# Kernel tuning notes

Measured on AMD Instinct MI355X. Metric: run time of the kernel, lower is better.

Reference implementation:

```python
import jax, jax.numpy as jnp
import numpy as np

ALG_DIM = 248   # dim of E8 adjoint rep
NNZ = 30000     # number of nonzero structure constants f_{ij}^k
BATCH = 8192


def setup_inputs() -> dict:
    key = jax.random.key(0)
    k1, k2, k3, k4, k5, k6 = jax.random.split(key, 6)
    x = jax.random.normal(k1, (BATCH, ALG_DIM), dtype=jnp.float32)
    y = jax.random.normal(k2, (BATCH, ALG_DIM), dtype=jnp.float32)
    idx_i = jax.random.randint(k3, (NNZ,), 0, ALG_DIM, dtype=jnp.int32)
    idx_j = jax.random.randint(k4, (NNZ,), 0, ALG_DIM, dtype=jnp.int32)
    idx_k = jax.random.randint(k5, (NNZ,), 0, ALG_DIM, dtype=jnp.int32)
    coeff = jax.random.normal(k6, (NNZ,), dtype=jnp.float32)
    alpha = jnp.ones((1,), dtype=jnp.float32)
    return {"x": x, "y": y, "idx_i": idx_i, "idx_j": idx_j,
            "idx_k": idx_k, "coeff": coeff, "alpha": alpha}


def reference(x, y, idx_i, idx_j, idx_k, coeff, alpha):
    # Sparse Lie bracket via structure-constant triples:
    #   out[b, k] = sum_{t : idx_k[t]==k} coeff[t] * x[b, idx_i[t]] * y[b, idx_j[t]]
    vals = x[:, idx_i] * y[:, idx_j] * coeff[None, :]          # (B, nnz)
    bracket = jnp.zeros_like(x).at[:, idx_k].add(vals)          # (B, 248)
    return alpha[0] * bracket
```

## Files before the change

### kernel.cpp

```cpp
#include <hip/hip_runtime.h>

#define ALG_DIM 248
#define ROWS 32
#define KSPLIT 4
#define KPB 62
#define PMAX 1024
#define CB 16
#define PLSTRIDE_B 3984
#define PLSTRIDE_DW 996

typedef __fp16 h2v __attribute__((ext_vector_type(2)));
union H2U { unsigned u; h2v h; };


__global__ __launch_bounds__(1024) void k_prep(
    const int* __restrict__ idx_k, int* __restrict__ meta,
    int* __restrict__ perm, int* __restrict__ ssz,
    int* __restrict__ coff, int* __restrict__ glim,
    uint2* __restrict__ packedP, int nnz)
{
    __shared__ int h[CB * 256];
    __shared__ int sz[256];
    __shared__ int ssl[256];
    __shared__ int red[256];
    const int tid = threadIdx.x;

    for (int u = tid; u < CB * 256; u += 1024) h[u] = 0;
    __syncthreads();

    const int w = tid >> 6, lane = tid & 63;
    const int chunk = (nnz + CB - 1) / CB;
    const int lo = w * chunk, hi = min(nnz, lo + chunk);
    for (int t = lo + lane; t < hi; t += 64)
        atomicAdd(&h[(w << 8) + idx_k[t]], 1);
    __syncthreads();

    if (tid < 256) {
        int tot = 0;
        for (int b = 0; b < CB; ++b) tot += h[b * 256 + tid];
        sz[tid] = (tid < ALG_DIM) ? tot : 0;
        red[tid] = sz[tid];
    }
    __syncthreads();
    for (int off = 128; off > 0; off >>= 1) {
        if (tid < off) red[tid] = max(red[tid], red[tid + off]);
        __syncthreads();
    }
    int P = (red[0] + 7) & ~7;
    P = max(P, 8);
    P = min(P, PMAX);
    if (tid == 0) meta[0] = P;
    const int stride = P + 8;

    int rank = 0, mysz = 0;
    if (tid < ALG_DIM) {
        mysz = sz[tid];
        for (int k = 0; k < ALG_DIM; ++k) {
            int s2 = sz[k];
            rank += (s2 > mysz) || (s2 == mysz && k < tid);
        }
        perm[rank] = tid;
        ssz[rank]  = mysz;
        ssl[rank]  = mysz;
        const int base = rank * stride;
        glim[tid] = base + P;
        int run = base;
        for (int b = 0; b < CB; ++b) {
            coff[b * 256 + tid] = run;
            run += h[b * 256 + tid];
        }
    }
    __syncthreads();
    if (tid < ALG_DIM) {
        const int by = rank / KPB;
        const int L  = by * KPB + (((rank - by * KPB) >> 4) << 4);
        const int trip = (ssl[L] + 7) & ~7;
        const int base = rank * stride;
        for (int e = mysz; e < trip + 8; ++e)
            packedP[base + e] = make_uint2(0u, 0u);
    }
}


__global__ void k_scatter(const int* __restrict__ idx_i, const int* __restrict__ idx_j,
                          const int* __restrict__ idx_k, const float* __restrict__ coeff,
                          const int* __restrict__ coff, const int* __restrict__ glim,
                          uint2* __restrict__ packedP, int nnz) {
    __shared__ int cur[256];
    __shared__ int lim[256];
    const int b = blockIdx.x, tid = threadIdx.x;
    cur[tid] = coff[b * 256 + tid];
    lim[tid] = glim[tid];
    __syncthreads();
    const int chunk = (nnz + CB - 1) / CB;
    const int lo = b * chunk, hi = min(nnz, lo + chunk);
    for (int t = lo + tid; t < hi; t += 256) {
        const int k = idx_k[t];
        const int pos = atomicAdd(&cur[k], 1);
        if (pos < lim[k]) {
            const float c = coeff[t];
            H2U hc; hc.h = __builtin_amdgcn_cvt_pkrtz(c, c);
            uint2 p;
            p.x = ((unsigned)idx_i[t] << 4) | ((unsigned)idx_j[t] << 20);
            p.y = hc.u;
            packedP[pos] = p;
        }
    }
}


__global__ __launch_bounds__(256, 4) void k_main(
    const float* __restrict__ x, const float* __restrict__ y,
    const uint4* __restrict__ packed4,
    const int* __restrict__ meta, const int* __restrict__ perm,
    const int* __restrict__ ssz,
    const float* __restrict__ alpha_p, float* __restrict__ out)
{
    __shared__ __align__(16) unsigned xs32[4 * PLSTRIDE_DW];
    __shared__ __align__(16) unsigned ys32[4 * PLSTRIDE_DW];

    const int tid = threadIdx.x;
    const int r0  = blockIdx.x * ROWS;

    for (int u = tid; u < (ALG_DIM / 4) * (ROWS / 2); u += 256) {
        const int rp = u & 15;
        const int cq = u >> 4;
        const size_t ra = (size_t)(r0 + 2 * rp) * ALG_DIM + 4 * cq;
        const float4 xa = *reinterpret_cast<const float4*>(x + ra);
        const float4 xb = *reinterpret_cast<const float4*>(x + ra + ALG_DIM);
        const float4 ya = *reinterpret_cast<const float4*>(y + ra);
        const float4 yb = *reinterpret_cast<const float4*>(y + ra + ALG_DIM);
        const int pbase = (rp >> 2) * PLSTRIDE_DW + (rp & 3);
#define STG(d, XA, XB, YA, YB)                                                  \
        {                                                                       \
            const int dw = pbase + (4 * cq + (d)) * 4;                          \
            H2U hx; hx.h = __builtin_amdgcn_cvt_pkrtz(XA, XB);                  \
            H2U hy; hy.h = __builtin_amdgcn_cvt_pkrtz(YA, YB);                  \
            xs32[dw] = hx.u;                                                    \
            ys32[dw] = hy.u;                                                    \
        }
        STG(0, xa.x, xb.x, ya.x, yb.x)
        STG(1, xa.y, xb.y, ya.y, yb.y)
        STG(2, xa.z, xb.z, ya.z, yb.z)
        STG(3, xa.w, xb.w, ya.w, yb.w)
#undef STG
    }
    __syncthreads();

    const int   P     = meta[0];
    const float alpha = alpha_p[0];
    const int   S     = tid >> 2;
    const int   q     = tid & 3;

    const char* xsb = reinterpret_cast<const char*>(xs32) + q * PLSTRIDE_B;
    const char* ysb = reinterpret_cast<const char*>(ys32) + q * PLSTRIDE_B;

    if (S < KPB) {
        const int p = blockIdx.y * KPB + S;
        const int k = perm[p];

        const int pw   = blockIdx.y * KPB + ((tid >> 6) << 4);
        const int trip = __builtin_amdgcn_readfirstlane((ssz[pw] + 7) & ~7);
        const int nH   = trip >> 1;

        const uint4* tp = packed4 + (size_t)p * ((size_t)(P + 8) >> 1);

        float a0 = 0.f, a1 = 0.f, a2 = 0.f, a3 = 0.f,
              a4 = 0.f, a5 = 0.f, a6 = 0.f, a7 = 0.f;

        uint4 cur = tp[0];

#define PROC(PW, PC)                                                            \
        {                                                                       \
            const unsigned ox = (PW) & 0xFFFFu;                                 \
            const unsigned oy = (PW) >> 16;                                     \
            const uint4 wx = *reinterpret_cast<const uint4*>(xsb + ox);         \
            const uint4 wy = *reinterpret_cast<const uint4*>(ysb + oy);         \
            H2U cc; cc.u = (PC);                                                \
            H2U ux, uy;                                                         \
            ux.u = wx.x; uy.u = wy.x; c0 = (ux.h * uy.h) * cc.h + c0;           \
            ux.u = wx.y; uy.u = wy.y; c1 = (ux.h * uy.h) * cc.h + c1;           \
            ux.u = wx.z; uy.u = wy.z; c2 = (ux.h * uy.h) * cc.h + c2;           \
            ux.u = wx.w; uy.u = wy.w; c3 = (ux.h * uy.h) * cc.h + c3;           \
        }

        for (int ch = 0; ch < nH; ch += 16) {
            h2v c0 = (h2v)0.0f, c1 = (h2v)0.0f, c2 = (h2v)0.0f, c3 = (h2v)0.0f;
            const int hend = min(ch + 16, nH);
#pragma unroll 2
            for (int hh = ch; hh < hend; ++hh) {
                const uint4 nxt = tp[hh + 1];
                PROC(cur.x, cur.y)
                PROC(cur.z, cur.w)
                cur = nxt;
            }
            a0 += (float)c0.x; a1 += (float)c0.y;
            a2 += (float)c1.x; a3 += (float)c1.y;
            a4 += (float)c2.x; a5 += (float)c2.y;
            a6 += (float)c3.x; a7 += (float)c3.y;
        }
#undef PROC

        const int rbase = r0 + (q << 3);
        out[(size_t)(rbase + 0) * ALG_DIM + k] = alpha * a0;
        out[(size_t)(rbase + 1) * ALG_DIM + k] = alpha * a1;
        out[(size_t)(rbase + 2) * ALG_DIM + k] = alpha * a2;
        out[(size_t)(rbase + 3) * ALG_DIM + k] = alpha * a3;
        out[(size_t)(rbase + 4) * ALG_DIM + k] = alpha * a4;
        out[(size_t)(rbase + 5) * ALG_DIM + k] = alpha * a5;
        out[(size_t)(rbase + 6) * ALG_DIM + k] = alpha * a6;
        out[(size_t)(rbase + 7) * ALG_DIM + k] = alpha * a7;
    }
}


extern "C" void kernel_launch(void* const* d_in, const int* in_sizes, int n_in,
                              void* d_out, int out_size, void* d_ws, size_t ws_size,
                              hipStream_t stream) {
    const float* x      = (const float*)d_in[0];
    const float* y      = (const float*)d_in[1];
    const int*   idx_i  = (const int*)d_in[2];
    const int*   idx_j  = (const int*)d_in[3];
    const int*   idx_k  = (const int*)d_in[4];
    const float* coeff  = (const float*)d_in[5];
    const float* alpha  = (const float*)d_in[6];
    float*       out    = (float*)d_out;

    const int nnz   = in_sizes[2];
    const int batch = in_sizes[0] / ALG_DIM;

    char*  ws      = (char*)d_ws;
    int*   meta    = (int*)ws;
    int*   perm    = (int*)(ws + 1024);
    int*   ssz     = (int*)(ws + 2048);
    int*   glim    = (int*)(ws + 3072);
    int*   coff    = (int*)(ws + 4096);
    uint2* packedP = (uint2*)(ws + 4096 + CB * 256 * 4 + 4096);

    k_prep   <<<1, 1024, 0, stream>>>(idx_k, meta, perm, ssz, coff, glim,
                                      packedP, nnz);
    k_scatter<<<CB, 256, 0, stream>>>(idx_i, idx_j, idx_k, coeff, coff, glim,
                                      packedP, nnz);

    dim3 grid(batch / ROWS, KSPLIT);
    k_main<<<grid, 256, 0, stream>>>(x, y, (const uint4*)packedP, meta, perm, ssz,
                                     alpha, out);
}
```

Before: 130.1 us.

## Fuse histogram prep and scatter into one redundant-per-block kernel

Merges the single-block histogram/sort kernel and the scatter kernel into one launch of CB blocks. Each block recomputes the full idx_k histogram and its own prefix count, then scatters its chunk directly. Block 0 additionally writes the metadata and zero padding. This removes one kernel launch and the global coff/glim round-trip, at the cost of every block redundantly scanning all nnz indices.

```diff
diff --git a/kernel.cpp b/kernel.cpp
--- a/kernel.cpp
+++ b/kernel.cpp
@@ -5,7 +5,7 @@
 #define KSPLIT 4
 #define KPB 62
 #define PMAX 1024
-#define CB 16
+#define CB 32
 #define PLSTRIDE_B 3984
 #define PLSTRIDE_DW 996
 
@@ -13,34 +13,35 @@
 union H2U { unsigned u; h2v h; };
 
 
-__global__ __launch_bounds__(1024) void k_prep(
-    const int* __restrict__ idx_k, int* __restrict__ meta,
-    int* __restrict__ perm, int* __restrict__ ssz,
-    int* __restrict__ coff, int* __restrict__ glim,
+__global__ __launch_bounds__(256) void k_prep2(
+    const int* __restrict__ idx_i, const int* __restrict__ idx_j,
+    const int* __restrict__ idx_k, const float* __restrict__ coeff,
+    int* __restrict__ meta, int* __restrict__ perm, int* __restrict__ ssz,
     uint2* __restrict__ packedP, int nnz)
 {
-    __shared__ int h[CB * 256];
-    __shared__ int sz[256];
+    __shared__ int htot[256];
+    __shared__ int hpre[256];
+    __shared__ int red[256];
     __shared__ int ssl[256];
-    __shared__ int red[256];
-    const int tid = threadIdx.x;
-
-    for (int u = tid; u < CB * 256; u += 1024) h[u] = 0;
-    __syncthreads();
-
-    const int w = tid >> 6, lane = tid & 63;
+    __shared__ int cur[256];
+    __shared__ int lim[256];
+
+    const int b = blockIdx.x, tid = threadIdx.x;
     const int chunk = (nnz + CB - 1) / CB;
-    const int lo = w * chunk, hi = min(nnz, lo + chunk);
-    for (int t = lo + lane; t < hi; t += 64)
-        atomicAdd(&h[(w << 8) + idx_k[t]], 1);
-    __syncthreads();
-
-    if (tid < 256) {
-        int tot = 0;
-        for (int b = 0; b < CB; ++b) tot += h[b * 256 + tid];
-        sz[tid] = (tid < ALG_DIM) ? tot : 0;
-        red[tid] = sz[tid];
-    }
+    const int lo = b * chunk, hi = min(nnz, lo + chunk);
+
+    htot[tid] = 0;
+    hpre[tid] = 0;
+    __syncthreads();
+
+    for (int t = tid; t < nnz; t += 256) {
+        const int k = idx_k[t];
+        atomicAdd(&htot[k], 1);
+        if (t < lo) atomicAdd(&hpre[k], 1);
+    }
+    __syncthreads();
+
+    red[tid] = (tid < ALG_DIM) ? htot[tid] : 0;
     __syncthreads();
     for (int off = 128; off > 0; off >>= 1) {
         if (tid < off) red[tid] = max(red[tid], red[tid + off]);
@@ -49,51 +50,39 @@
     int P = (red[0] + 7) & ~7;
     P = max(P, 8);
     P = min(P, PMAX);
-    if (tid == 0) meta[0] = P;
     const int stride = P + 8;
 
     int rank = 0, mysz = 0;
     if (tid < ALG_DIM) {
-        mysz = sz[tid];
+        mysz = htot[tid];
         for (int k = 0; k < ALG_DIM; ++k) {
-            int s2 = sz[k];
+            const int s2 = htot[k];
             rank += (s2 > mysz) || (s2 == mysz && k < tid);
         }
-        perm[rank] = tid;
-        ssz[rank]  = mysz;
-        ssl[rank]  = mysz;
         const int base = rank * stride;
-        glim[tid] = base + P;
-        int run = base;
-        for (int b = 0; b < CB; ++b) {
-            coff[b * 256 + tid] = run;
-            run += h[b * 256 + tid];
-        }
-    }
-    __syncthreads();
-    if (tid < ALG_DIM) {
-        const int by = rank / KPB;
-        const int L  = by * KPB + (((rank - by * KPB) >> 4) << 4);
-        const int trip = (ssl[L] + 7) & ~7;
-        const int base = rank * stride;
-        for (int e = mysz; e < trip + 8; ++e)
-            packedP[base + e] = make_uint2(0u, 0u);
-    }
-}
-
-
-__global__ void k_scatter(const int* __restrict__ idx_i, const int* __restrict__ idx_j,
-                          const int* __restrict__ idx_k, const float* __restrict__ coeff,
-                          const int* __restrict__ coff, const int* __restrict__ glim,
-                          uint2* __restrict__ packedP, int nnz) {
-    __shared__ int cur[256];
-    __shared__ int lim[256];
-    const int b = blockIdx.x, tid = threadIdx.x;
-    cur[tid] = coff[b * 256 + tid];
-    lim[tid] = glim[tid];
-    __syncthreads();
-    const int chunk = (nnz + CB - 1) / CB;
-    const int lo = b * chunk, hi = min(nnz, lo + chunk);
+        cur[tid] = base + hpre[tid];
+        lim[tid] = base + P;
+    }
+
+    if (b == 0) {
+        if (tid == 0) meta[0] = P;
+        if (tid < ALG_DIM) {
+            perm[rank] = tid;
+            ssz[rank]  = mysz;
+            ssl[rank]  = mysz;
+        }
+        __syncthreads();
+        if (tid < ALG_DIM) {
+            const int by = rank / KPB;
+            const int L  = by * KPB + (((rank - by * KPB) >> 4) << 4);
+            const int trip = (ssl[L] + 7) & ~7;
+            const int base = rank * stride;
+            for (int e = mysz; e < trip + 8; ++e)
+                packedP[base + e] = make_uint2(0u, 0u);
+        }
+    }
+    __syncthreads();
+
     for (int t = lo + tid; t < hi; t += 256) {
         const int k = idx_k[t];
         const int pos = atomicAdd(&cur[k], 1);
@@ -233,14 +222,10 @@
     int*   meta    = (int*)ws;
     int*   perm    = (int*)(ws + 1024);
     int*   ssz     = (int*)(ws + 2048);
-    int*   glim    = (int*)(ws + 3072);
-    int*   coff    = (int*)(ws + 4096);
-    uint2* packedP = (uint2*)(ws + 4096 + CB * 256 * 4 + 4096);
-
-    k_prep   <<<1, 1024, 0, stream>>>(idx_k, meta, perm, ssz, coff, glim,
-                                      packedP, nnz);
-    k_scatter<<<CB, 256, 0, stream>>>(idx_i, idx_j, idx_k, coeff, coff, glim,
-                                      packedP, nnz);
+    uint2* packedP = (uint2*)(ws + 4096);
+
+    k_prep2<<<CB, 256, 0, stream>>>(idx_i, idx_j, idx_k, coeff,
+                                    meta, perm, ssz, packedP, nnz);
 
     dim3 grid(batch / ROWS, KSPLIT);
     k_main<<<grid, 256, 0, stream>>>(x, y, (const uint4*)packedP, meta, perm, ssz,
```

After: 145.4 us. +11.8%, slower.
